# Kernel tuning notes

Measured on AMD Instinct MI355X. Metric: run time of the kernel, lower is better.

The kernel has to match this reference:

```python
import jax, jax.numpy as jnp
import numpy as np

HEADS = 8
DIM_HEAD = 64


def setup_inputs() -> dict:
    key = jax.random.key(0)
    ks = jax.random.split(key, 7)
    b, c, h, w = 8, 256, 64, 64
    hidden = HEADS * DIM_HEAD  # 512
    return {
        "x": jax.random.normal(ks[0], (b, c, h, w), dtype=jnp.float32),
        "context": jax.random.normal(ks[1], (b, c, h, w), dtype=jnp.float32),
        "Wq": jax.random.normal(ks[2], (hidden, c), dtype=jnp.float32) * 0.02,
        "Wk": jax.random.normal(ks[3], (hidden, c), dtype=jnp.float32) * 0.02,
        "Wv": jax.random.normal(ks[4], (hidden, c), dtype=jnp.float32) * 0.02,
        "Wo": jax.random.normal(ks[5], (c, hidden), dtype=jnp.float32) * 0.02,
        "bo": jnp.zeros((c,), dtype=jnp.float32),
    }


def reference(x, context, Wq, Wk, Wv, Wo, bo):
    b, c, h, w = x.shape
    n = h * w
    scale = DIM_HEAD ** (-0.5)
    xf = x.reshape(b, c, n)                      # b c n
    cf = context.reshape(b, context.shape[1], -1)  # b c m
    # 1x1 convs == per-pixel linear projections
    q = jnp.einsum('bcn,oc->bon', xf, Wq).reshape(b, HEADS, DIM_HEAD, n) * scale
    k = jnp.einsum('bcm,oc->bom', cf, Wk).reshape(b, HEADS, DIM_HEAD, -1)
    v = jnp.einsum('bcm,oc->bom', cf, Wv).reshape(b, HEADS, DIM_HEAD, -1)
    k = jax.nn.softmax(k, axis=-1)               # softmax over spatial positions
    ctx = jnp.einsum('bhdm,bhem->bhde', k, v)    # small d x e context
    out = jnp.einsum('bhde,bhdn->bhen', ctx, q)  # b h e n
    out = out.reshape(b, HEADS * DIM_HEAD, h, w)
    return jnp.einsum('bchw,oc->bohw', out, Wo) + bo[None, :, None, None]
```

## Files before the change

kernel.cpp:

```cpp
#include <hip/hip_runtime.h>

#define B   8
#define C   256
#define N   4096
#define H   8
#define D   64
#define HID 512
#define SCALE 0.125f

typedef __attribute__((ext_vector_type(8))) __bf16 bf16x8;
typedef __attribute__((ext_vector_type(4))) float f32x4;

__device__ __forceinline__ ushort bfbits(float f) {
  union { __bf16 h; ushort u; } c; c.h = (__bf16)f; return c.u;
}

__device__ __forceinline__ f32x4 mfma16(bf16x8 a, bf16x8 b, f32x4 c) {
  return __builtin_amdgcn_mfma_f32_16x16x32_bf16(a, b, c, 0, 0, 0);
}

__device__ __forceinline__ void glds16(const ushort* g, ushort* l) {
  __builtin_amdgcn_global_load_lds(
      (const __attribute__((address_space(1))) void*)g,
      (__attribute__((address_space(3))) void*)l, 16, 0, 0);
}

__global__ __launch_bounds__(256) void prep_kernel(
    const float* __restrict__ x, const float* __restrict__ ctxt,
    const float* __restrict__ Wk, const float* __restrict__ Wv,
    ushort* __restrict__ x_bf, ushort* __restrict__ ctxt_bf,
    ushort* __restrict__ wk_bf, ushort* __restrict__ wv_bf) {
  const int z = blockIdx.z;
  const int tid = threadIdx.x;
  if (z == 16) {
    const int id = blockIdx.y * 64 + blockIdx.x;
    if (id >= 128) return;
    const int t = (id * 256 + tid) * 4;
    const float4 a = *(const float4*)(Wk + t);
    const float4 b = *(const float4*)(Wv + t);
    ushort4 ra, rb;
    ra.x = bfbits(a.x); ra.y = bfbits(a.y); ra.z = bfbits(a.z); ra.w = bfbits(a.w);
    rb.x = bfbits(b.x); rb.y = bfbits(b.y); rb.z = bfbits(b.z); rb.w = bfbits(b.w);
    *(ushort4*)(wk_bf + t) = ra;
    *(ushort4*)(wv_bf + t) = rb;
    return;
  }
  __shared__ float tile[64 * 65];
  const int b = z & 7;
  const float* src = (z < 8) ? ctxt : x;
  ushort* dst = (z < 8) ? ctxt_bf : x_bf;
  const int l0 = blockIdx.x * 64, r0 = blockIdx.y * 64;
  const int rr = tid >> 4, c4 = (tid & 15) << 2;
  const float* sp = src + ((size_t)b * C + r0) * N + l0;
#pragma unroll
  for (int p = 0; p < 4; ++p) {
    const float4 v = *(const float4*)(sp + (size_t)(rr + p * 16) * N + c4);
    float* tp = tile + (rr + p * 16) * 65 + c4;
    tp[0] = v.x; tp[1] = v.y; tp[2] = v.z; tp[3] = v.w;
  }
  __syncthreads();
  const int lr = tid >> 2, rb = (tid & 3) << 4;
  uint pk[8];
#pragma unroll
  for (int k = 0; k < 16; k += 2) {
    const uint lo = bfbits(tile[(rb + k) * 65 + lr]);
    const uint hi = bfbits(tile[(rb + k + 1) * 65 + lr]);
    pk[k >> 1] = lo | (hi << 16);
  }
  ushort* dp = dst + ((size_t)b * N + l0 + lr) * C + r0 + rb;
  *(uint4*)dp = *(uint4*)pk;
  *(uint4*)(dp + 8) = *(uint4*)(pk + 4);
}

__global__ __launch_bounds__(256, 4) void kv_mfma_kernel(
    const ushort* __restrict__ ctxt_bf,
    const ushort* __restrict__ wk_bf,
    const ushort* __restrict__ wv_bf,
    float* __restrict__ ctx_part,
    float* __restrict__ z_part)
{
  __shared__ __align__(16) ushort cb_s[2][32 * 256];
  __shared__ __align__(16) ushort p_s[64 * 32];
  __shared__ __align__(16) ushort v_s[64 * 32];
  const int mt = blockIdx.x, h = blockIdx.y, b = blockIdx.z;
  const int tid = threadIdx.x;
  const int w = tid >> 6, lane = tid & 63;
  const int col = lane & 15, quad = lane >> 4;
  const int dw = w * 16;
  const int swc = (col & 3) ^ ((col >> 2) & 3);

  const ushort* wkp = wk_bf + (size_t)(h * 64 + dw + col) * C + quad * 8;
  const ushort* wvp = wv_bf + (size_t)(h * 64 + dw + col) * C + quad * 8;
  const ushort* cbase = ctxt_bf + ((size_t)b * N + (size_t)mt * 256) * C;

  bf16x8 wkf[8], wvf[8];
#pragma unroll
  for (int kk = 0; kk < 8; ++kk) {
    wkf[kk] = *(const bf16x8*)(wkp + (size_t)kk * 32);
    wvf[kk] = *(const bf16x8*)(wvp + (size_t)kk * 32);
  }

  const int grow0 = w * 8 + (lane >> 5);
  const int ggran = lane & 31;

  const f32x4 z4 = {0.f, 0.f, 0.f, 0.f};
  f32x4 cacc[4];
#pragma unroll
  for (int j = 0; j < 4; ++j) cacc[j] = z4;
  float zl = 0.f;

#pragma unroll
  for (int it = 0; it < 4; ++it) {
    const int row = grow0 + it * 2;
    glds16(cbase + (size_t)row * C + ((ggran ^ (row & 7)) << 3),
           &cb_s[0][(w * 8 + it * 2) * 256]);
  }
  __syncthreads();

  for (int t = 0; t < 8; ++t) {
    const int cur = t & 1;
    if (t < 7) {
      const ushort* nb = cbase + (size_t)(t + 1) * 32 * C;
#pragma unroll
      for (int it = 0; it < 4; ++it) {
        const int row = grow0 + it * 2;
        glds16(nb + (size_t)row * C + ((ggran ^ (row & 7)) << 3),
               &cb_s[cur ^ 1][(w * 8 + it * 2) * 256]);
      }
    }

    f32x4 kacc[2], vacc[2];
#pragma unroll
    for (int i = 0; i < 2; ++i) { kacc[i] = z4; vacc[i] = z4; }
    __builtin_amdgcn_s_setprio(1);
#pragma unroll
    for (int kk = 0; kk < 8; ++kk) {
      bf16x8 a[2];
#pragma unroll
      for (int i = 0; i < 2; ++i) {
        const int r = i * 16 + col;
        a[i] = *(const bf16x8*)(&cb_s[cur][r * 256 +
                  ((((kk << 2) + quad) ^ (r & 7)) << 3)]);
      }
#pragma unroll
      for (int i = 0; i < 2; ++i) {
        kacc[i] = mfma16(a[i], wkf[kk], kacc[i]);
        vacc[i] = mfma16(a[i], wvf[kk], vacc[i]);
      }
    }
    __builtin_amdgcn_s_setprio(0);

#pragma unroll
    for (int i = 0; i < 2; ++i) {
      const int off = (dw + col) * 32 +
                      (((i * 2 + (quad >> 1)) ^ swc) << 3) + ((quad & 1) << 2);
      const f32x4 k4 = kacc[i];
      const float e0 = __expf(k4[0]), e1 = __expf(k4[1]);
      const float e2 = __expf(k4[2]), e3 = __expf(k4[3]);
      zl += (e0 + e1) + (e2 + e3);
      ushort4 pk; pk.x = bfbits(e0); pk.y = bfbits(e1);
      pk.z = bfbits(e2); pk.w = bfbits(e3);
      *(ushort4*)(p_s + off) = pk;
      const f32x4 v4 = vacc[i];
      ushort4 vk; vk.x = bfbits(v4[0]); vk.y = bfbits(v4[1]);
      vk.z = bfbits(v4[2]); vk.w = bfbits(v4[3]);
      *(ushort4*)(v_s + off) = vk;
    }
    __syncthreads();

    {
      const int g = (quad ^ swc) << 3;
      const bf16x8 pa = *(const bf16x8*)(p_s + (dw + col) * 32 + g);
      bf16x8 vb[4];
#pragma unroll
      for (int j = 0; j < 4; ++j)
        vb[j] = *(const bf16x8*)(v_s + (j * 16 + col) * 32 + g);
      __builtin_amdgcn_s_setprio(1);
#pragma unroll
      for (int j = 0; j < 4; ++j) cacc[j] = mfma16(pa, vb[j], cacc[j]);
      __builtin_amdgcn_s_setprio(0);
    }
    __syncthreads();
  }

  {
    float s = zl;
    s += __shfl_xor(s, 16); s += __shfl_xor(s, 32);
    if (quad == 0)
      z_part[((size_t)(b * H + h) * 16 + mt) * 64 + dw + col] = s;
  }

  float* outp = ctx_part + ((size_t)(b * H + h) * 16 + mt) * 4096;
#pragma unroll
  for (int j = 0; j < 4; ++j)
#pragma unroll
    for (int r = 0; r < 4; ++r)
      outp[(size_t)(dw + quad * 4 + r) * 64 + j * 16 + col] = cacc[j][r];
}

__global__ __launch_bounds__(256) void combine_kernel(
    const float* __restrict__ ctx_part, const float* __restrict__ z_part,
    float* __restrict__ ctxn)
{
  const int bh = blockIdx.x, seg = blockIdx.y, tid = threadIdx.x;
  __shared__ float zs[64];
  if (tid < 64) {
    float z = 0.f;
#pragma unroll
    for (int p = 0; p < 16; ++p) z += z_part[((size_t)bh * 16 + p) * 64 + tid];
    zs[tid] = SCALE / z;
  }
  __syncthreads();
  const int idx = (seg << 8) + tid;
  const float* cp = ctx_part + (size_t)bh * 16 * 4096;
  float s = 0.f;
#pragma unroll
  for (int p = 0; p < 16; ++p) s += cp[(size_t)p * 4096 + idx];
  ctxn[((size_t)bh << 12) + idx] = s * zs[idx >> 6];
}

__global__ __launch_bounds__(256) void a_kernel(
    const float* __restrict__ ctxn, const float* __restrict__ Wq,
    float* __restrict__ A)
{
  const int bh = blockIdx.x, cti = blockIdx.y, tid = threadIdx.x;
  const int b = bh >> 3, h = bh & 7;
  const int c0 = cti << 6;
  __shared__ float ct[64 * 65];
  __shared__ float wq[64 * 68];
  for (int r = 0; r < 16; ++r) {
    const int idx = tid + (r << 8);
    ct[(idx & 63) * 65 + (idx >> 6)] = ctxn[((size_t)bh << 12) + idx];
    wq[(idx >> 6) * 68 + (idx & 63)] =
        Wq[(size_t)(h * 64 + (idx >> 6)) * C + c0 + (idx & 63)];
  }
  __syncthreads();
  const int e = tid & 63, co = tid >> 6;
  float acc[16];
#pragma unroll
  for (int k = 0; k < 16; ++k) acc[k] = 0.f;
  for (int d = 0; d < 64; ++d) {
    const float cv = ct[e * 65 + d];
    const float* wr = wq + d * 68 + co * 16;
#pragma unroll
    for (int k = 0; k < 16; ++k) acc[k] += cv * wr[k];
  }
  float* Ar = A + ((size_t)b * HID + h * 64 + e) * C + c0 + co * 16;
#pragma unroll
  for (int k = 0; k < 16; ++k) Ar[k] = acc[k];
}

__global__ __launch_bounds__(256) void m_kernel(
    const float* __restrict__ A, const float* __restrict__ Wo,
    ushort* __restrict__ M_bf)
{
  const int tile = blockIdx.x, b = blockIdx.y;
  const int o0 = (tile & 7) << 5, c0 = (tile >> 3) << 6;
  const int tid = threadIdx.x, tx = tid & 15, ty = tid >> 4;
  __shared__ float wo_s[64 * 33];
  __shared__ float a_s[64 * 68];
  float acc[2][4] = {{0.f}};
  const int wo_o = tid >> 3, wo_k = (tid & 7) << 3;
  const int a_k = tid >> 2, a_c = (tid & 3) << 4;
  float4 wr0, wr1, ar0, ar1, ar2, ar3;
  {
    const float* wp = Wo + (size_t)(o0 + wo_o) * HID + wo_k;
    wr0 = *(const float4*)wp; wr1 = *(const float4*)(wp + 4);
    const float* ap = A + ((size_t)b * HID + a_k) * C + c0 + a_c;
    ar0 = *(const float4*)ap;       ar1 = *(const float4*)(ap + 4);
    ar2 = *(const float4*)(ap + 8); ar3 = *(const float4*)(ap + 12);
  }
  for (int t = 0; t < 8; ++t) {
    __syncthreads();
    {
      float* wd = wo_s + wo_k * 33 + wo_o;
      wd[0]   = wr0.x; wd[33]  = wr0.y; wd[66]  = wr0.z; wd[99]  = wr0.w;
      wd[132] = wr1.x; wd[165] = wr1.y; wd[198] = wr1.z; wd[231] = wr1.w;
      float* ad = a_s + a_k * 68 + a_c;
      *(float4*)ad = ar0;       *(float4*)(ad + 4) = ar1;
      *(float4*)(ad + 8) = ar2; *(float4*)(ad + 12) = ar3;
    }
    __syncthreads();
    if (t < 7) {
      const int k0 = (t + 1) << 6;
      const float* wp = Wo + (size_t)(o0 + wo_o) * HID + k0 + wo_k;
      wr0 = *(const float4*)wp; wr1 = *(const float4*)(wp + 4);
      const float* ap = A + ((size_t)b * HID + k0 + a_k) * C + c0 + a_c;
      ar0 = *(const float4*)ap;       ar1 = *(const float4*)(ap + 4);
      ar2 = *(const float4*)(ap + 8); ar3 = *(const float4*)(ap + 12);
    }
#pragma unroll
    for (int kc = 0; kc < 64; ++kc) {
      const float2 wv = *(const float2*)(wo_s + kc * 33 + ty * 2);
      const float4 av = *(const float4*)(a_s + kc * 68 + tx * 4);
      acc[0][0] += wv.x * av.x; acc[0][1] += wv.x * av.y;
      acc[0][2] += wv.x * av.z; acc[0][3] += wv.x * av.w;
      acc[1][0] += wv.y * av.x; acc[1][1] += wv.y * av.y;
      acc[1][2] += wv.y * av.z; acc[1][3] += wv.y * av.w;
    }
  }
#pragma unroll
  for (int i = 0; i < 2; ++i) {
    ushort4 r;
    r.x = bfbits(acc[i][0]); r.y = bfbits(acc[i][1]);
    r.z = bfbits(acc[i][2]); r.w = bfbits(acc[i][3]);
    *(ushort4*)(M_bf + ((size_t)b * C + o0 + ty * 2 + i) * C + c0 + tx * 4) = r;
  }
}

__global__ __launch_bounds__(256, 4) void out_mfma_kernel(
    const ushort* __restrict__ M_bf,
    const ushort* __restrict__ x_bf,
    const float* __restrict__ bo, float* __restrict__ out)
{
  const int r = blockIdx.x + 16 * blockIdx.y + 128 * blockIdx.z;
  const int xcd = r & 7, slot = r >> 3;
  const int grp = xcd * 16 + (slot >> 3);
  const int ot = slot & 7;
  const int b = grp >> 4, nt = grp & 15;
  const int tid = threadIdx.x;
  const int w = tid >> 6, lane = tid & 63;
  const int col = lane & 15, quad = lane >> 4;
  const int o0 = ot * 32;
  const size_t n_base = (size_t)nt * 256 + w * 64;
  const ushort* Ab = M_bf + ((size_t)b * C + o0 + col) * C + quad * 8;
  const ushort* Bb = x_bf + ((size_t)b * N + n_base) * C + quad * 8;

  const f32x4 z4 = {0.f, 0.f, 0.f, 0.f};
  f32x4 acc[2][4];
#pragma unroll
  for (int i = 0; i < 2; ++i)
#pragma unroll
    for (int j = 0; j < 4; ++j) acc[i][j] = z4;

#pragma unroll
  for (int kk = 0; kk < 8; ++kk) {
    bf16x8 af[2], bfz[4];
#pragma unroll
    for (int i = 0; i < 2; ++i)
      af[i] = *(const bf16x8*)(Ab + (size_t)(i * 16) * C + kk * 32);
#pragma unroll
    for (int j = 0; j < 4; ++j)
      bfz[j] = *(const bf16x8*)(Bb + (size_t)(j * 16 + col) * C + kk * 32);
#pragma unroll
    for (int i = 0; i < 2; ++i)
#pragma unroll
      for (int j = 0; j < 4; ++j) acc[i][j] = mfma16(af[i], bfz[j], acc[i][j]);
  }

#pragma unroll
  for (int i = 0; i < 2; ++i)
#pragma unroll
    for (int r2 = 0; r2 < 4; ++r2) {
      const int o = o0 + i * 16 + quad * 4 + r2;
      const float bias = bo[o];
      float* op = out + ((size_t)b * C + o) * N + n_base + col;
#pragma unroll
      for (int j = 0; j < 4; ++j) op[j * 16] = acc[i][j][r2] + bias;
    }
}

extern "C" void kernel_launch(void* const* d_in, const int* in_sizes, int n_in,
                              void* d_out, int out_size, void* d_ws, size_t ws_size,
                              hipStream_t stream) {
  const float* x    = (const float*)d_in[0];
  const float* ctxt = (const float*)d_in[1];
  const float* Wq   = (const float*)d_in[2];
  const float* Wk   = (const float*)d_in[3];
  const float* Wv   = (const float*)d_in[4];
  const float* Wo   = (const float*)d_in[5];
  const float* bo   = (const float*)d_in[6];
  float* out = (float*)d_out;

  char* p = (char*)d_ws;
  ushort* ctxt_bf = (ushort*)p;  p += (size_t)B * N * C * 2;
  ushort* x_bf    = (ushort*)p;  p += (size_t)B * N * C * 2;
  ushort* wk_bf   = (ushort*)p;  p += (size_t)HID * C * 2;
  ushort* wv_bf   = (ushort*)p;  p += (size_t)HID * C * 2;
  ushort* M_bf    = (ushort*)p;  p += (size_t)B * C * C * 2;
  float*  z_part  = (float*)p;   p += (size_t)B * H * 16 * 64 * 4;
  float*  ctxn    = (float*)p;   p += (size_t)B * H * D * D * 4;
  float*  ctx_part= (float*)p;   p += (size_t)B * H * 16 * 4096 * 4;
  float*  A       = ctx_part;

  prep_kernel<<<dim3(N / 64, C / 64, 17), 256, 0, stream>>>(
      x, ctxt, Wk, Wv, x_bf, ctxt_bf, wk_bf, wv_bf);
  kv_mfma_kernel<<<dim3(16, H, B), 256, 0, stream>>>(
      ctxt_bf, wk_bf, wv_bf, ctx_part, z_part);
  combine_kernel<<<dim3(B * H, 16), 256, 0, stream>>>(ctx_part, z_part, ctxn);
  a_kernel<<<dim3(B * H, 4), 256, 0, stream>>>(ctxn, Wq, A);
  m_kernel<<<dim3(32, B), 256, 0, stream>>>(A, Wo, M_bf);
  out_mfma_kernel<<<dim3(N / 256, C / 32, B), 256, 0, stream>>>(M_bf, x_bf, bo, out);
}
```

Before: 237.1 us.

## Double-buffer P/V tiles to drop a barrier, stream weight fragments from global

Double-buffers the P and V shared tiles in the KV kernel so that each iteration writes the current chunk while running the P·V MFMA on the previous chunk. This removes one __syncthreads per iteration and adds a tail step after the loop. The Wk/Wv fragments are no longer preloaded into registers; they are reloaded from global memory inside the inner k loop, which cuts register pressure. The occupancy hint drops from 4 to 3 blocks per SM. The trade is extra global or L2 traffic for the weights and lower occupancy, in exchange for fewer barriers and lighter register use.

```diff
diff --git a/kernel.cpp b/kernel.cpp
--- a/kernel.cpp
+++ b/kernel.cpp
@@ -72,7 +72,7 @@
   *(uint4*)(dp + 8) = *(uint4*)(pk + 4);
 }
 
-__global__ __launch_bounds__(256, 4) void kv_mfma_kernel(
+__global__ __launch_bounds__(256, 3) void kv_mfma_kernel(
     const ushort* __restrict__ ctxt_bf,
     const ushort* __restrict__ wk_bf,
     const ushort* __restrict__ wv_bf,
@@ -80,8 +80,8 @@
     float* __restrict__ z_part)
 {
   __shared__ __align__(16) ushort cb_s[2][32 * 256];
-  __shared__ __align__(16) ushort p_s[64 * 32];
-  __shared__ __align__(16) ushort v_s[64 * 32];
+  __shared__ __align__(16) ushort p_s[2][64 * 32];
+  __shared__ __align__(16) ushort v_s[2][64 * 32];
   const int mt = blockIdx.x, h = blockIdx.y, b = blockIdx.z;
   const int tid = threadIdx.x;
   const int w = tid >> 6, lane = tid & 63;
@@ -93,13 +93,6 @@
   const ushort* wvp = wv_bf + (size_t)(h * 64 + dw + col) * C + quad * 8;
   const ushort* cbase = ctxt_bf + ((size_t)b * N + (size_t)mt * 256) * C;
 
-  bf16x8 wkf[8], wvf[8];
-#pragma unroll
-  for (int kk = 0; kk < 8; ++kk) {
-    wkf[kk] = *(const bf16x8*)(wkp + (size_t)kk * 32);
-    wvf[kk] = *(const bf16x8*)(wvp + (size_t)kk * 32);
-  }
-
   const int grow0 = w * 8 + (lane >> 5);
   const int ggran = lane & 31;
 
@@ -142,10 +135,12 @@
         a[i] = *(const bf16x8*)(&cb_s[cur][r * 256 +
                   ((((kk << 2) + quad) ^ (r & 7)) << 3)]);
       }
+      const bf16x8 wkf = *(const bf16x8*)(wkp + (size_t)kk * 32);
+      const bf16x8 wvf = *(const bf16x8*)(wvp + (size_t)kk * 32);
 #pragma unroll
       for (int i = 0; i < 2; ++i) {
-        kacc[i] = mfma16(a[i], wkf[kk], kacc[i]);
-        vacc[i] = mfma16(a[i], wvf[kk], vacc[i]);
+        kacc[i] = mfma16(a[i], wkf, kacc[i]);
+        vacc[i] = mfma16(a[i], wvf, vacc[i]);
       }
     }
     __builtin_amdgcn_s_setprio(0);
@@ -160,27 +155,37 @@
       zl += (e0 + e1) + (e2 + e3);
       ushort4 pk; pk.x = bfbits(e0); pk.y = bfbits(e1);
       pk.z = bfbits(e2); pk.w = bfbits(e3);
-      *(ushort4*)(p_s + off) = pk;
+      *(ushort4*)(&p_s[cur][off]) = pk;
       const f32x4 v4 = vacc[i];
       ushort4 vk; vk.x = bfbits(v4[0]); vk.y = bfbits(v4[1]);
       vk.z = bfbits(v4[2]); vk.w = bfbits(v4[3]);
-      *(ushort4*)(v_s + off) = vk;
-    }
-    __syncthreads();
-
-    {
+      *(ushort4*)(&v_s[cur][off]) = vk;
+    }
+
+    if (t > 0) {
       const int g = (quad ^ swc) << 3;
-      const bf16x8 pa = *(const bf16x8*)(p_s + (dw + col) * 32 + g);
+      const bf16x8 pa = *(const bf16x8*)(&p_s[cur ^ 1][(dw + col) * 32 + g]);
       bf16x8 vb[4];
 #pragma unroll
       for (int j = 0; j < 4; ++j)
-        vb[j] = *(const bf16x8*)(v_s + (j * 16 + col) * 32 + g);
+        vb[j] = *(const bf16x8*)(&v_s[cur ^ 1][(j * 16 + col) * 32 + g]);
       __builtin_amdgcn_s_setprio(1);
 #pragma unroll
       for (int j = 0; j < 4; ++j) cacc[j] = mfma16(pa, vb[j], cacc[j]);
       __builtin_amdgcn_s_setprio(0);
     }
     __syncthreads();
+  }
+
+  {
+    const int g = (quad ^ swc) << 3;
+    const bf16x8 pa = *(const bf16x8*)(&p_s[1][(dw + col) * 32 + g]);
+    bf16x8 vb[4];
+#pragma unroll
+    for (int j = 0; j < 4; ++j)
+      vb[j] = *(const bf16x8*)(&v_s[1][(j * 16 + col) * 32 + g]);
+#pragma unroll
+    for (int j = 0; j < 4; ++j) cacc[j] = mfma16(pa, vb[j], cacc[j]);
   }
 
   {
```

New measurement: 247.2 us. 4.3% more time.
